# Kernel tuning notes

Measured on AMD Instinct MI355X. Metric: run time of the kernel, lower is better.

## Reference

```python
import jax, jax.numpy as jnp
import numpy as np

N_NODES = 50000
N_EDGES = 800000
C = 64          # node channels (in_dim == out_dim)
CE = 32         # edge channels
NEG_SLOPE = 0.2


def setup_inputs() -> dict:
    key = jax.random.key(0)
    k1, k2, k3, k4, k5 = jax.random.split(key, 5)
    x = jax.random.normal(k1, (N_NODES, C), dtype=jnp.float32)
    edge_index = jax.random.randint(k2, (2, N_EDGES), 0, N_NODES, dtype=jnp.int64)
    edge_attr = jax.random.normal(k3, (N_EDGES, CE), dtype=jnp.float32)
    # parameters (kaiming-uniform-ish scale)
    wn_bound = float(np.sqrt(6.0 / C))
    weight_node = jax.random.uniform(k4, (C, C), minval=-wn_bound, maxval=wn_bound, dtype=jnp.float32)
    wa_bound = float(np.sqrt(6.0 / (2 * C + CE)))
    weight_triplet_att = jax.random.uniform(k5, (1, 2 * C + CE), minval=-wa_bound, maxval=wa_bound, dtype=jnp.float32)
    bias = jnp.zeros((C,), dtype=jnp.float32)
    return {"x": x, "edge_index": edge_index, "edge_attr": edge_attr,
            "weight_node": weight_node, "weight_triplet_att": weight_triplet_att, "bias": bias}


def reference(x, edge_index, edge_attr, weight_node, weight_triplet_att, bias):
    # x: [N, C], edge_index: [2, E] (row 0 = source j, row 1 = target i), edge_attr: [E, Ce]
    n_nodes = x.shape[0]
    xw = x @ weight_node                      # [N, C]
    src, dst = edge_index[0], edge_index[1]
    x_j = xw[src]                             # [E, C] messages from source
    x_i = xw[dst]                             # [E, C] target features
    triplet = jnp.concatenate([x_i, edge_attr, x_j], axis=-1)   # [E, 2C+Ce]
    alpha = (triplet * weight_triplet_att).sum(axis=-1)          # [E]
    alpha = jax.nn.leaky_relu(alpha, NEG_SLOPE)
    # segment softmax over edges grouped by destination node (PyG softmax)
    seg_max = jax.ops.segment_max(alpha, dst, num_segments=n_nodes)  # [N]
    alpha = jnp.exp(alpha - seg_max[dst])
    seg_sum = jax.ops.segment_sum(alpha, dst, num_segments=n_nodes)  # [N]
    alpha = alpha / (seg_sum[dst] + 1e-16)
    msg = alpha[:, None] * x_j                                      # [E, C]
    out = jax.ops.segment_sum(msg, dst, num_segments=n_nodes)       # [N, C]
    return out + bias
```

## Files before the change

kernel.cpp:

```cpp
#include <hip/hip_runtime.h>
#include <math.h>

#define N_NODES 50000
#define N_EDGES 800000
#define C 64
#define CE 32
#define NEG_SLOPE 0.2f

#define SLOT 64
#define SLOT_SHIFT 6

#define BN 128
#define BN_SHIFT 7
#define NB ((N_NODES + BN - 1) / BN)
#define NB_PAD 448
#define TILE 1024
#define EPT (TILE / 256)
#define CAP 2560
#define GC_STRIDE 16

#define K1_BLOCKS 1024
#define NROWG ((N_NODES + 3) / 4)

__device__ __forceinline__ unsigned bf16_rne(float f) {
    unsigned u = __float_as_uint(f);
    return (u + 0x7FFFu + ((u >> 16) & 1u)) >> 16;
}

__global__ __launch_bounds__(256) void k1_xw(
    const float* __restrict__ x, const float* __restrict__ W,
    const float* __restrict__ watt,
    unsigned short* __restrict__ xwb, float* __restrict__ a_i, float* __restrict__ a_j,
    unsigned* __restrict__ gcur)
{
    int lane = threadIdx.x & 63;
    int warp = threadIdx.x >> 6;
    if (blockIdx.x == 0)
        for (int i = threadIdx.x; i < NB * GC_STRIDE; i += 256) gcur[i] = 0u;
    float Wc[64];
#pragma unroll
    for (int k = 0; k < 64; k++) Wc[k] = W[k * 64 + lane];
    float wi = watt[lane], wj = watt[96 + lane];
    for (int rg = blockIdx.x; rg < NROWG; rg += gridDim.x) {
        int row = rg * 4 + warp;
        if (row >= N_NODES) continue;
        float xv = x[(size_t)row * C + lane];
        float acc = 0.f;
#pragma unroll
        for (int k = 0; k < 64; k++) {
            float xs = __int_as_float(__builtin_amdgcn_readlane(__float_as_int(xv), k));
            acc = fmaf(xs, Wc[k], acc);
        }
        xwb[(size_t)row * C + lane] = (unsigned short)bf16_rne(acc);
        float vi = acc * wi;
        float vj = acc * wj;
#pragma unroll
        for (int off = 32; off; off >>= 1) {
            vi += __shfl_down(vi, off, 64);
            vj += __shfl_down(vj, off, 64);
        }
        if (lane == 0) { a_i[row] = vi; a_j[row] = vj; }
    }
}

__global__ __launch_bounds__(256) void k2_bin(
    const int* __restrict__ eidx, const float* __restrict__ edge_attr,
    const float* __restrict__ watt,
    const float* __restrict__ a_i, const float* __restrict__ a_j,
    unsigned* __restrict__ gcur, uint2* __restrict__ bbuf)
{
    __shared__ uint2 pay[TILE];
    __shared__ unsigned hcnt[NB_PAD], lbase[NB_PAD], lcur[NB_PAD], gb[NB_PAD];
    int tid = threadIdx.x;
    size_t tb = (size_t)blockIdx.x * TILE;
    for (int i = tid; i < NB_PAD; i += 256) hcnt[i] = 0u;
    __syncthreads();

    unsigned pkv[EPT], dstv[EPT];
#pragma unroll
    for (int k = 0; k < EPT; k++) {
        size_t e = tb + (size_t)k * 256 + tid;
        bool ok = e < (size_t)N_EDGES;
        size_t ee = ok ? e : 0;
        int src = eidx[ee];
        int dst = eidx[N_EDGES + ee];
        const float4* ea = (const float4*)(edge_attr + ee * CE);
        float ec = 0.f;
#pragma unroll
        for (int q = 0; q < CE / 4; q++) {
            float4 v = ea[q];
            ec += v.x * watt[64 + 4 * q + 0] + v.y * watt[64 + 4 * q + 1] +
                  v.z * watt[64 + 4 * q + 2] + v.w * watt[64 + 4 * q + 3];
        }
        float al = a_i[dst] + ec + a_j[src];
        al = al > 0.f ? al : NEG_SLOPE * al;
        pkv[k] = ((unsigned)src << 16) | bf16_rne(__expf(al));
        dstv[k] = ok ? (unsigned)dst : 0xFFFFFFFFu;
        if (ok) atomicAdd(&hcnt[(unsigned)dst >> BN_SHIFT], 1u);
    }
    __syncthreads();

    if (tid < 64) {
        unsigned carry = 0u;
        for (int cch = 0; cch < 7; cch++) {
            unsigned v = hcnt[cch * 64 + tid];
            unsigned inc = v;
#pragma unroll
            for (int off = 1; off < 64; off <<= 1) {
                unsigned t = __shfl_up(inc, off, 64);
                if (tid >= off) inc += t;
            }
            unsigned excl = carry + inc - v;
            lbase[cch * 64 + tid] = excl;
            lcur[cch * 64 + tid] = excl;
            carry += (unsigned)__shfl((int)inc, 63, 64);
        }
    }
    __syncthreads();

    for (int b = tid; b < NB; b += 256) {
        unsigned h = hcnt[b];
        gb[b] = h ? atomicAdd(&gcur[b * GC_STRIDE], h) : 0u;
    }
    __syncthreads();

#pragma unroll
    for (int k = 0; k < EPT; k++) {
        if (dstv[k] != 0xFFFFFFFFu) {
            unsigned b = dstv[k] >> BN_SHIFT;
            unsigned p = atomicAdd(&lcur[b], 1u);
            pay[p] = make_uint2(pkv[k], dstv[k]);
        }
    }
    __syncthreads();

    unsigned total = lbase[NB_PAD - 1];
    for (unsigned i = tid; i < total; i += 256) {
        uint2 v = pay[i];
        unsigned b = v.y >> BN_SHIFT;
        unsigned gpos = gb[b] + (i - lbase[b]);
        if (gpos < (unsigned)CAP)
            bbuf[(size_t)b * CAP + gpos] = v;
    }
}

__global__ __launch_bounds__(256) void k3_rank(
    const unsigned* __restrict__ gcur, const uint2* __restrict__ bbuf,
    unsigned* __restrict__ count, unsigned* __restrict__ sorted)
{
    __shared__ unsigned lcnt[BN];
    int b = blockIdx.x, tid = threadIdx.x;
    if (tid < BN) lcnt[tid] = 0u;
    __syncthreads();
    unsigned tot = gcur[b * GC_STRIDE];
    tot = tot > (unsigned)CAP ? (unsigned)CAP : tot;
    const uint2* seg = bbuf + (size_t)b * CAP;
    for (unsigned i = tid; i < tot; i += 256) {
        uint2 v = seg[i];
        unsigned ln = v.y & (BN - 1);
        unsigned r = atomicAdd(&lcnt[ln], 1u);
        if (r < (unsigned)SLOT)
            sorted[((size_t)v.y << SLOT_SHIFT) + r] = v.x;
    }
    __syncthreads();
    if (tid < BN) {
        unsigned node = ((unsigned)b << BN_SHIFT) + tid;
        if (node < N_NODES) {
            unsigned c = lcnt[tid];
            count[node] = c > (unsigned)SLOT ? (unsigned)SLOT : c;
        }
    }
}

__global__ __launch_bounds__(256) void k5_gather(
    const unsigned* __restrict__ count, const unsigned* __restrict__ sorted,
    const unsigned short* __restrict__ xwb, const float* __restrict__ bias,
    float* __restrict__ out)
{
    int warp = threadIdx.x >> 6, lane = threadIdx.x & 63;
    int node = blockIdx.x * 4 + warp;
    if (node >= N_NODES) return;
    int group = lane >> 3, sub = lane & 7;
    unsigned c = count[node];
    unsigned pk = 0u;
    if (lane < (int)c) pk = sorted[((unsigned)node << SLOT_SHIFT) + lane];
    float wpart = __uint_as_float(pk << 16);
    float acc[8];
#pragma unroll
    for (int i = 0; i < 8; i++) acc[i] = 0.f;
    unsigned iters = (c + 7) >> 3;
    for (unsigned it = 0; it < iters; it++) {
        int t = (int)(it * 8) + group;
        unsigned p = (unsigned)__shfl((int)pk, t, 64);
        float w = __uint_as_float(p << 16);
        unsigned s = p >> 16;
        uint4 v = ((const uint4*)(xwb + (size_t)s * C))[sub];
        acc[0] += w * __uint_as_float(v.x << 16);
        acc[1] += w * __uint_as_float(v.x & 0xFFFF0000u);
        acc[2] += w * __uint_as_float(v.y << 16);
        acc[3] += w * __uint_as_float(v.y & 0xFFFF0000u);
        acc[4] += w * __uint_as_float(v.z << 16);
        acc[5] += w * __uint_as_float(v.z & 0xFFFF0000u);
        acc[6] += w * __uint_as_float(v.w << 16);
        acc[7] += w * __uint_as_float(v.w & 0xFFFF0000u);
    }
#pragma unroll
    for (int off = 8; off < 64; off <<= 1) {
#pragma unroll
        for (int i = 0; i < 8; i++) acc[i] += __shfl_xor(acc[i], off, 64);
    }
#pragma unroll
    for (int off = 1; off < 64; off <<= 1)
        wpart += __shfl_xor(wpart, off, 64);
    float rden = 1.0f / (wpart + 1e-16f);
    if (group == 0) {
        float4 b4a = ((const float4*)bias)[sub * 2];
        float4 b4b = ((const float4*)bias)[sub * 2 + 1];
        float4 o1, o2;
        o1.x = acc[0] * rden + b4a.x; o1.y = acc[1] * rden + b4a.y;
        o1.z = acc[2] * rden + b4a.z; o1.w = acc[3] * rden + b4a.w;
        o2.x = acc[4] * rden + b4b.x; o2.y = acc[5] * rden + b4b.y;
        o2.z = acc[6] * rden + b4b.z; o2.w = acc[7] * rden + b4b.w;
        ((float4*)(out + (size_t)node * C))[sub * 2] = o1;
        ((float4*)(out + (size_t)node * C))[sub * 2 + 1] = o2;
    }
}

extern "C" void kernel_launch(void* const* d_in, const int* in_sizes, int n_in,
                              void* d_out, int out_size, void* d_ws, size_t ws_size,
                              hipStream_t stream) {
    const float* x         = (const float*)d_in[0];
    const int*   eidx      = (const int*)d_in[1];
    const float* edge_attr = (const float*)d_in[2];
    const float* W         = (const float*)d_in[3];
    const float* watt      = (const float*)d_in[4];
    const float* bias      = (const float*)d_in[5];
    float* out = (float*)d_out;

    char* ws = (char*)d_ws;
    size_t off = 0;
    auto alloc = [&](size_t bytes) -> void* {
        void* p = ws + off;
        off += (bytes + 255) & ~(size_t)255;
        return p;
    };
    unsigned short* xwb  = (unsigned short*)alloc((size_t)N_NODES * C * 2);
    float*    a_i    = (float*)alloc(N_NODES * 4);
    float*    a_j    = (float*)alloc(N_NODES * 4);
    unsigned* gcur   = (unsigned*)alloc((size_t)NB * GC_STRIDE * 4);
    uint2*    bbuf   = (uint2*)alloc((size_t)NB * CAP * 8);
    unsigned* count  = (unsigned*)alloc(N_NODES * 4);
    unsigned* sorted = (unsigned*)alloc((size_t)N_NODES * SLOT * 4);

    k1_xw<<<K1_BLOCKS, 256, 0, stream>>>(x, W, watt, xwb, a_i, a_j, gcur);
    k2_bin<<<(N_EDGES + TILE - 1) / TILE, 256, 0, stream>>>(eidx, edge_attr, watt,
                                                            a_i, a_j, gcur, bbuf);
    k3_rank<<<NB, 256, 0, stream>>>(gcur, bbuf, count, sorted);
    k5_gather<<<(N_NODES + 3) / 4, 256, 0, stream>>>(count, sorted, xwb, bias, out);
}
```

Baseline: 249.2 us.

## Scatter edges directly to global bins and move softmax weight computation into rank kernel

The binning kernel drops its local prefix scan and shared staging buffer and writes each edge straight to its global bin slot with a shared atomic cursor. It now carries the partial logit (edge term plus source term) and the packed src/dst key. The a_i lookup, leaky-relu and exp move into the rank kernel, which also accumulates the per-node denominator in full precision. The gather kernel reads this denominator instead of reducing bf16 weights across the wave. Bins double to 256 nodes, and k1 reads x rows through scalar loads with four independent accumulators. The cost is uncoalesced global scatter writes in k2 and float atomics in LDS during ranking.

```diff
diff --git a/kernel.cpp b/kernel.cpp
--- a/kernel.cpp
+++ b/kernel.cpp
@@ -10,13 +10,12 @@
 #define SLOT 64
 #define SLOT_SHIFT 6
 
-#define BN 128
-#define BN_SHIFT 7
+#define BN 256
+#define BN_SHIFT 8
 #define NB ((N_NODES + BN - 1) / BN)
-#define NB_PAD 448
 #define TILE 1024
 #define EPT (TILE / 256)
-#define CAP 2560
+#define CAP 5120
 #define GC_STRIDE 16
 
 #define K1_BLOCKS 1024
@@ -44,13 +43,18 @@
     for (int rg = blockIdx.x; rg < NROWG; rg += gridDim.x) {
         int row = rg * 4 + warp;
         if (row >= N_NODES) continue;
-        float xv = x[(size_t)row * C + lane];
-        float acc = 0.f;
-#pragma unroll
-        for (int k = 0; k < 64; k++) {
-            float xs = __int_as_float(__builtin_amdgcn_readlane(__float_as_int(xv), k));
-            acc = fmaf(xs, Wc[k], acc);
-        }
+        int row_u = __builtin_amdgcn_readfirstlane(row);
+        const float* xr = x + (size_t)row_u * C;
+        float a0 = 0.f, a1 = 0.f, a2 = 0.f, a3 = 0.f;
+#pragma unroll
+        for (int k = 0; k < 64; k += 4) {
+            float s0 = xr[k], s1 = xr[k + 1], s2 = xr[k + 2], s3 = xr[k + 3];
+            a0 = fmaf(s0, Wc[k],     a0);
+            a1 = fmaf(s1, Wc[k + 1], a1);
+            a2 = fmaf(s2, Wc[k + 2], a2);
+            a3 = fmaf(s3, Wc[k + 3], a3);
+        }
+        float acc = (a0 + a1) + (a2 + a3);
         xwb[(size_t)row * C + lane] = (unsigned short)bf16_rne(acc);
         float vi = acc * wi;
         float vj = acc * wj;
@@ -65,18 +69,16 @@
 
 __global__ __launch_bounds__(256) void k2_bin(
     const int* __restrict__ eidx, const float* __restrict__ edge_attr,
-    const float* __restrict__ watt,
-    const float* __restrict__ a_i, const float* __restrict__ a_j,
+    const float* __restrict__ watt, const float* __restrict__ a_j,
     unsigned* __restrict__ gcur, uint2* __restrict__ bbuf)
 {
-    __shared__ uint2 pay[TILE];
-    __shared__ unsigned hcnt[NB_PAD], lbase[NB_PAD], lcur[NB_PAD], gb[NB_PAD];
+    __shared__ unsigned hcnt[NB], gslot[NB];
     int tid = threadIdx.x;
     size_t tb = (size_t)blockIdx.x * TILE;
-    for (int i = tid; i < NB_PAD; i += 256) hcnt[i] = 0u;
-    __syncthreads();
-
-    unsigned pkv[EPT], dstv[EPT];
+    for (int i = tid; i < NB; i += 256) hcnt[i] = 0u;
+    __syncthreads();
+
+    float av[EPT]; unsigned key[EPT];
 #pragma unroll
     for (int k = 0; k < EPT; k++) {
         size_t e = tb + (size_t)k * 256 + tid;
@@ -92,88 +94,69 @@
             ec += v.x * watt[64 + 4 * q + 0] + v.y * watt[64 + 4 * q + 1] +
                   v.z * watt[64 + 4 * q + 2] + v.w * watt[64 + 4 * q + 3];
         }
-        float al = a_i[dst] + ec + a_j[src];
-        al = al > 0.f ? al : NEG_SLOPE * al;
-        pkv[k] = ((unsigned)src << 16) | bf16_rne(__expf(al));
-        dstv[k] = ok ? (unsigned)dst : 0xFFFFFFFFu;
+        av[k] = ec + a_j[src];
+        key[k] = ok ? (((unsigned)src << 16) | (unsigned)dst) : 0xFFFFFFFFu;
         if (ok) atomicAdd(&hcnt[(unsigned)dst >> BN_SHIFT], 1u);
-    }
-    __syncthreads();
-
-    if (tid < 64) {
-        unsigned carry = 0u;
-        for (int cch = 0; cch < 7; cch++) {
-            unsigned v = hcnt[cch * 64 + tid];
-            unsigned inc = v;
-#pragma unroll
-            for (int off = 1; off < 64; off <<= 1) {
-                unsigned t = __shfl_up(inc, off, 64);
-                if (tid >= off) inc += t;
-            }
-            unsigned excl = carry + inc - v;
-            lbase[cch * 64 + tid] = excl;
-            lcur[cch * 64 + tid] = excl;
-            carry += (unsigned)__shfl((int)inc, 63, 64);
-        }
     }
     __syncthreads();
 
     for (int b = tid; b < NB; b += 256) {
         unsigned h = hcnt[b];
-        gb[b] = h ? atomicAdd(&gcur[b * GC_STRIDE], h) : 0u;
+        gslot[b] = h ? atomicAdd(&gcur[b * GC_STRIDE], h) : 0u;
     }
     __syncthreads();
 
 #pragma unroll
     for (int k = 0; k < EPT; k++) {
-        if (dstv[k] != 0xFFFFFFFFu) {
-            unsigned b = dstv[k] >> BN_SHIFT;
-            unsigned p = atomicAdd(&lcur[b], 1u);
-            pay[p] = make_uint2(pkv[k], dstv[k]);
-        }
-    }
-    __syncthreads();
-
-    unsigned total = lbase[NB_PAD - 1];
-    for (unsigned i = tid; i < total; i += 256) {
-        uint2 v = pay[i];
-        unsigned b = v.y >> BN_SHIFT;
-        unsigned gpos = gb[b] + (i - lbase[b]);
-        if (gpos < (unsigned)CAP)
-            bbuf[(size_t)b * CAP + gpos] = v;
+        if (key[k] != 0xFFFFFFFFu) {
+            unsigned b = (key[k] & 0xFFFFu) >> BN_SHIFT;
+            unsigned slot = atomicAdd(&gslot[b], 1u);
+            if (slot < (unsigned)CAP)
+                bbuf[(size_t)b * CAP + slot] = make_uint2(__float_as_uint(av[k]), key[k]);
+        }
     }
 }
 
 __global__ __launch_bounds__(256) void k3_rank(
     const unsigned* __restrict__ gcur, const uint2* __restrict__ bbuf,
-    unsigned* __restrict__ count, unsigned* __restrict__ sorted)
+    const float* __restrict__ a_i,
+    unsigned* __restrict__ count, float* __restrict__ den,
+    unsigned* __restrict__ sorted)
 {
     __shared__ unsigned lcnt[BN];
+    __shared__ float lden[BN];
     int b = blockIdx.x, tid = threadIdx.x;
-    if (tid < BN) lcnt[tid] = 0u;
+    lcnt[tid] = 0u; lden[tid] = 0.f;
     __syncthreads();
     unsigned tot = gcur[b * GC_STRIDE];
     tot = tot > (unsigned)CAP ? (unsigned)CAP : tot;
     const uint2* seg = bbuf + (size_t)b * CAP;
     for (unsigned i = tid; i < tot; i += 256) {
         uint2 v = seg[i];
-        unsigned ln = v.y & (BN - 1);
+        unsigned dst = v.y & 0xFFFFu;
+        unsigned src = v.y >> 16;
+        float al = a_i[dst] + __uint_as_float(v.x);
+        al = al > 0.f ? al : NEG_SLOPE * al;
+        float w = __expf(al);
+        unsigned ln = dst & (BN - 1);
         unsigned r = atomicAdd(&lcnt[ln], 1u);
-        if (r < (unsigned)SLOT)
-            sorted[((size_t)v.y << SLOT_SHIFT) + r] = v.x;
-    }
-    __syncthreads();
-    if (tid < BN) {
-        unsigned node = ((unsigned)b << BN_SHIFT) + tid;
-        if (node < N_NODES) {
-            unsigned c = lcnt[tid];
-            count[node] = c > (unsigned)SLOT ? (unsigned)SLOT : c;
-        }
+        if (r < (unsigned)SLOT) {
+            sorted[((size_t)dst << SLOT_SHIFT) + r] = (src << 16) | bf16_rne(w);
+            atomicAdd(&lden[ln], w);
+        }
+    }
+    __syncthreads();
+    unsigned node = ((unsigned)b << BN_SHIFT) + tid;
+    if (node < N_NODES) {
+        unsigned c = lcnt[tid];
+        count[node] = c > (unsigned)SLOT ? (unsigned)SLOT : c;
+        den[node] = lden[tid];
     }
 }
 
 __global__ __launch_bounds__(256) void k5_gather(
-    const unsigned* __restrict__ count, const unsigned* __restrict__ sorted,
+    const unsigned* __restrict__ count, const float* __restrict__ den,
+    const unsigned* __restrict__ sorted,
     const unsigned short* __restrict__ xwb, const float* __restrict__ bias,
     float* __restrict__ out)
 {
@@ -184,7 +167,6 @@
     unsigned c = count[node];
     unsigned pk = 0u;
     if (lane < (int)c) pk = sorted[((unsigned)node << SLOT_SHIFT) + lane];
-    float wpart = __uint_as_float(pk << 16);
     float acc[8];
 #pragma unroll
     for (int i = 0; i < 8; i++) acc[i] = 0.f;
@@ -209,10 +191,7 @@
 #pragma unroll
         for (int i = 0; i < 8; i++) acc[i] += __shfl_xor(acc[i], off, 64);
     }
-#pragma unroll
-    for (int off = 1; off < 64; off <<= 1)
-        wpart += __shfl_xor(wpart, off, 64);
-    float rden = 1.0f / (wpart + 1e-16f);
+    float rden = 1.0f / (den[node] + 1e-16f);
     if (group == 0) {
         float4 b4a = ((const float4*)bias)[sub * 2];
         float4 b4b = ((const float4*)bias)[sub * 2 + 1];
@@ -250,11 +229,12 @@
     unsigned* gcur   = (unsigned*)alloc((size_t)NB * GC_STRIDE * 4);
     uint2*    bbuf   = (uint2*)alloc((size_t)NB * CAP * 8);
     unsigned* count  = (unsigned*)alloc(N_NODES * 4);
+    float*    den    = (float*)alloc(N_NODES * 4);
     unsigned* sorted = (unsigned*)alloc((size_t)N_NODES * SLOT * 4);
 
     k1_xw<<<K1_BLOCKS, 256, 0, stream>>>(x, W, watt, xwb, a_i, a_j, gcur);
     k2_bin<<<(N_EDGES + TILE - 1) / TILE, 256, 0, stream>>>(eidx, edge_attr, watt,
-                                                            a_i, a_j, gcur, bbuf);
-    k3_rank<<<NB, 256, 0, stream>>>(gcur, bbuf, count, sorted);
-    k5_gather<<<(N_NODES + 3) / 4, 256, 0, stream>>>(count, sorted, xwb, bias, out);
-}
+                                                            a_j, gcur, bbuf);
+    k3_rank<<<NB, 256, 0, stream>>>(gcur, bbuf, a_i, count, den, sorted);
+    k5_gather<<<(N_NODES + 3) / 4, 256, 0, stream>>>(count, den, sorted, xwb, bias, out);
+}
```

Result: no change. 251.0 us (+0.7%).
